# Optimization experiments

Hardware: AMD Instinct MI355X
Metric: run time of the kernel (lower is better)

The kernel has to match this reference:

```python
import jax, jax.numpy as jnp
import numpy as np

CUTOFF = 4          # lattice cutoff radius (module init arg)
NMAX = 64           # padded max neighbors per mobile site (~58 actual at cutoff=4)
BATCH = 131072      # number of independent configurations
B_SOFT = 0.01       # softening constant b in vint
FAR = 1e6           # padding position, masked out


def _rot(c):
    return np.array([[np.cos(c), -np.sin(c)], [np.sin(c), np.cos(c)]])


def _build_geometry():
    """Replicates PotEnergy1P.__init__ (with the intended, bug-fixed math)."""
    s3 = np.sqrt(3.0)
    base = [np.array([0.5, s3 / 6]), np.array([1.0, -s3 / 3]),
            np.array([1.5, s3 / 6]), np.array([1.0, 2 * s3 / 3])]
    mobile = base \
        + [_rot(2 * np.pi / 3) @ p for p in base] \
        + [_rot(4 * np.pi / 3) @ p for p in base]
    mobile = np.stack(mobile)                      # [12, 2]

    def ntopos(n1, n2):
        return np.array([0.5, s3 / 6]) + n1 * np.array([1.0, 0.0]) \
            + n2 * np.array([-0.5, s3 / 2])

    rng = range(-4 * CUTOFF, 4 * CUTOFF)
    grid = np.array([ntopos(n1, n2) for n1 in rng for n2 in rng])  # [G, 2]
    dist = np.linalg.norm(grid[:, None, :] - mobile[None, :, :], axis=-1)  # [G, 12]
    not_mobile = ~np.any(np.isclose(dist, 0.0, atol=1e-8), axis=1)        # [G]

    neighbors = np.full((12, NMAX, 2), FAR, dtype=np.float32)
    mask = np.zeros((12, NMAX), dtype=np.float32)
    for i in range(12):
        idx = np.where(not_mobile & (dist[:, i] < CUTOFF))[0]
        k = len(idx)
        assert k <= NMAX
        neighbors[i, :k] = grid[idx]
        mask[i, :k] = 1.0
    return neighbors, mask


def setup_inputs() -> dict:
    key = jax.random.key(0)
    x = jax.random.normal(key, (BATCH, 24), dtype=jnp.float32)
    neighbors, mask = _build_geometry()
    return {"x": x,
            "neighbors": jnp.asarray(neighbors),
            "mask": jnp.asarray(mask)}


def reference(x, neighbors, mask):
    # x: [B, 24] -> [B, 12, 2] mobile positions
    xr = x.reshape(x.shape[0], -1, 2)
    # pairwise displacement to all padded neighbors: [B, 12, NMAX, 2]
    d = xr[:, :, None, :] - neighbors[None, :, :, :]
    r = jnp.sqrt(jnp.sum(d * d, axis=-1))          # [B, 12, NMAX]
    v = jnp.exp(-r) / (r + B_SOFT)                 # vint with a=1.0, b=0.01
    return jnp.sum(v * mask[None], axis=(1, 2))    # [B] total potential energy
```

## Files before the change

### kernel.cpp

```cpp
#include <hip/hip_runtime.h>
#include <math.h>

#define NMAX   64
#define NSITES 12
#define SPLIT  4
#define BLOCK  256
#define RS     68

#define B_SOFT 0.01f
#define PAD_C  4.0e4f
#define R2_MAX 248.0f
#define TBL_LO 1392
#define TBL_N  768

#define NB_FLOATS  (NSITES * RS)
#define TBL_OFF    (TBL_LO * 8)
#define SMEM_BYTES (TBL_OFF + TBL_N * 8)

#define WS_TBL_F   1664
#define WS_FLOATS  3200
__device__ __align__(16) float g_ws[WS_FLOATS];
__device__ int g_m;

typedef float v2f __attribute__((ext_vector_type(2)));
typedef float v4f __attribute__((ext_vector_type(4)));

__device__ __forceinline__ float f_exact(float r2) {
    const float r = sqrtf(r2);
    return expf(-r) / (r + B_SOFT);
}

__global__ void init_kernel(const float* __restrict__ neighbors,
                            const float* __restrict__ mask) {
    __shared__ int cnt[NSITES];
    const int tid  = threadIdx.x;
    const int wv   = tid >> 6;
    const int lane = tid & 63;

    for (int i = tid; i < 2 * NB_FLOATS; i += BLOCK) g_ws[i] = PAD_C;
    __syncthreads();

    for (int s = wv; s < NSITES; s += 4) {
        const bool keep = mask[s * NMAX + lane] > 0.5f;
        const unsigned long long bal = __ballot(keep);
        if (keep) {
            const int pos = __popcll(bal & ((1ull << lane) - 1ull));
            const float2 p = ((const float2*)neighbors)[s * NMAX + lane];
            g_ws[s * RS + pos]             = p.x;
            g_ws[NB_FLOATS + s * RS + pos] = p.y;
        }
        if (lane == 0) cnt[s] = __popcll(bal);
    }
    __syncthreads();
    if (tid == 0) {
        int m = 0;
        #pragma unroll
        for (int s = 0; s < NSITES; ++s) m = max(m, cnt[s]);
        g_m = (m + 3) & ~3;
    }

    for (int i = tid; i < TBL_N; i += BLOCK) {
        const unsigned ii = (unsigned)(i + TBL_LO);
        const float b0 = __builtin_bit_cast(float, ii << 19);
        const float b1 = __builtin_bit_cast(float, (ii + 1u) << 19);
        const float f0 = f_exact(b0);
        const float f1 = f_exact(b1);
        const float fm = f_exact(0.5f * (b0 + b1));
        const float sl = (f1 - f0) / (b1 - b0);
        const float c  = f0 - sl * b0 - 0.5f * (0.5f * (f0 + f1) - fm);
        g_ws[WS_TBL_F + 2 * i]     = c;
        g_ws[WS_TBL_F + 2 * i + 1] = sl;
    }
}

__global__ __launch_bounds__(BLOCK, 8)
void pot_energy_kernel(const float* __restrict__ x,
                       float* __restrict__ out, int B) {
    __shared__ __align__(16) char smem[SMEM_BYTES];
    const int tid = threadIdx.x;

    {
        const float4* s0 = (const float4*)g_ws;
        float4* d0 = (float4*)smem;
        #pragma unroll
        for (int i = 0; i < 2; ++i) {
            const int idx = tid + i * BLOCK;
            if (idx < (2 * NB_FLOATS) / 4) d0[idx] = s0[idx];
        }
        const float4* s1 = (const float4*)(g_ws + WS_TBL_F);
        float4* d1 = (float4*)(smem + TBL_OFF);
        #pragma unroll
        for (int i = 0; i < 2; ++i) {
            const int idx = tid + i * BLOCK;
            if (idx < (TBL_N * 8) / 16) d1[idx] = s1[idx];
        }
    }
    const int m = g_m;
    __syncthreads();

    const int gtid = blockIdx.x * BLOCK + tid;
    const int e = gtid >> 2;
    const int q = gtid & 3;
    if (e >= B) return;

    const float2* xp = (const float2*)(x + (size_t)gtid * 6);
    const float2 p0 = xp[0], p1 = xp[1], p2 = xp[2];
    const float xs_[3] = { p0.x, p1.x, p2.x };
    const float ys_[3] = { p0.y, p1.y, p2.y };

    const float R2MINF = __builtin_bit_cast(float, 0x2B800000u);

    float accC = 0.f, accS = 0.f;
    #pragma unroll
    for (int s = 0; s < 3; ++s) {
        const int site = q * 3 + s;
        const float* __restrict__ rx = (const float*)smem + site * RS;
        const float* __restrict__ ry = rx + NB_FLOATS;
        const v2f xs2 = { xs_[s], xs_[s] };
        const v2f ys2 = { ys_[s], ys_[s] };
        #pragma unroll 2
        for (int j0 = 0; j0 < m; j0 += 4) {
            const v4f nx4 = *(const v4f*)(rx + j0);
            const v4f ny4 = *(const v4f*)(ry + j0);
            const v2f dxA = xs2 - nx4.xy;
            const v2f dxB = xs2 - nx4.zw;
            const v2f dyA = ys2 - ny4.xy;
            const v2f dyB = ys2 - ny4.zw;
            const v2f r2A = __builtin_elementwise_fma(dyA, dyA, dxA * dxA);
            const v2f r2B = __builtin_elementwise_fma(dyB, dyB, dxB * dxB);
            const float r2k[4] = { r2A.x, r2A.y, r2B.x, r2B.y };
            #pragma unroll
            for (int k = 0; k < 4; ++k) {
                const float r2c = __builtin_amdgcn_fmed3f(r2k[k], R2MINF, R2_MAX);
                const unsigned off =
                    (__builtin_bit_cast(unsigned, r2c) >> 16) & 0xFFF8u;
                const float2 cs = *(const float2*)(smem + off);
                accC += cs.x;
                accS = fmaf(cs.y, r2c, accS);
            }
        }
    }

    float acc = accC + accS;
    acc += __shfl_xor(acc, 1);
    acc += __shfl_xor(acc, 2);
    if (q == 0) out[e] = acc;
}

extern "C" void kernel_launch(void* const* d_in, const int* in_sizes, int n_in,
                              void* d_out, int out_size, void* d_ws, size_t ws_size,
                              hipStream_t stream) {
    const float* x   = (const float*)d_in[0];
    const float* nbr = (const float*)d_in[1];
    const float* msk = (const float*)d_in[2];
    float* out = (float*)d_out;

    const int B = in_sizes[0] / 24;

    init_kernel<<<1, BLOCK, 0, stream>>>(nbr, msk);

    const int total_threads = B * SPLIT;
    const int blocks = (total_threads + BLOCK - 1) / BLOCK;
    pot_energy_kernel<<<blocks, BLOCK, 0, stream>>>(x, out, B);
}
```

Baseline: 80.95 us.

## Replace piecewise-linear LDS lookup table with direct transcendental evaluation

Drops the precomputed interpolation table for exp(-r)/(r+b) indexed by r2 bits, and computes each pair term directly with hardware sqrt, exp2 and rcp intrinsics. This removes the per-pair LDS gather, with its possible bank conflicts, and the table build in the init kernel. In exchange each pair now issues three transcendental instructions, which run at reduced rate, and the packed v2f math is gone. Precision now relies on approximate rcp/exp instead of the table error.

After: 90.38 us. 1.12x slower.

```diff
diff --git a/kernel.cpp b/kernel.cpp
--- a/kernel.cpp
+++ b/kernel.cpp
@@ -9,26 +9,14 @@
 
 #define B_SOFT 0.01f
 #define PAD_C  4.0e4f
-#define R2_MAX 248.0f
-#define TBL_LO 1392
-#define TBL_N  768
 
-#define NB_FLOATS  (NSITES * RS)
-#define TBL_OFF    (TBL_LO * 8)
-#define SMEM_BYTES (TBL_OFF + TBL_N * 8)
+#define NB_FLOATS (NSITES * RS)
+#define WS_F      (2 * NB_FLOATS)
 
-#define WS_TBL_F   1664
-#define WS_FLOATS  3200
-__device__ __align__(16) float g_ws[WS_FLOATS];
+__device__ __align__(16) float g_ws[WS_F];
 __device__ int g_m;
 
-typedef float v2f __attribute__((ext_vector_type(2)));
 typedef float v4f __attribute__((ext_vector_type(4)));
-
-__device__ __forceinline__ float f_exact(float r2) {
-    const float r = sqrtf(r2);
-    return expf(-r) / (r + B_SOFT);
-}
 
 __global__ void init_kernel(const float* __restrict__ neighbors,
                             const float* __restrict__ mask) {
@@ -37,7 +25,7 @@
     const int wv   = tid >> 6;
     const int lane = tid & 63;
 
-    for (int i = tid; i < 2 * NB_FLOATS; i += BLOCK) g_ws[i] = PAD_C;
+    for (int i = tid; i < WS_F; i += BLOCK) g_ws[i] = PAD_C;
     __syncthreads();
 
     for (int s = wv; s < NSITES; s += 4) {
@@ -58,41 +46,21 @@
         for (int s = 0; s < NSITES; ++s) m = max(m, cnt[s]);
         g_m = (m + 3) & ~3;
     }
-
-    for (int i = tid; i < TBL_N; i += BLOCK) {
-        const unsigned ii = (unsigned)(i + TBL_LO);
-        const float b0 = __builtin_bit_cast(float, ii << 19);
-        const float b1 = __builtin_bit_cast(float, (ii + 1u) << 19);
-        const float f0 = f_exact(b0);
-        const float f1 = f_exact(b1);
-        const float fm = f_exact(0.5f * (b0 + b1));
-        const float sl = (f1 - f0) / (b1 - b0);
-        const float c  = f0 - sl * b0 - 0.5f * (0.5f * (f0 + f1) - fm);
-        g_ws[WS_TBL_F + 2 * i]     = c;
-        g_ws[WS_TBL_F + 2 * i + 1] = sl;
-    }
 }
 
 __global__ __launch_bounds__(BLOCK, 8)
 void pot_energy_kernel(const float* __restrict__ x,
                        float* __restrict__ out, int B) {
-    __shared__ __align__(16) char smem[SMEM_BYTES];
+    __shared__ __align__(16) float smem[WS_F];
     const int tid = threadIdx.x;
 
     {
-        const float4* s0 = (const float4*)g_ws;
-        float4* d0 = (float4*)smem;
+        const float4* s4 = (const float4*)g_ws;
+        float4* d4 = (float4*)smem;
         #pragma unroll
         for (int i = 0; i < 2; ++i) {
             const int idx = tid + i * BLOCK;
-            if (idx < (2 * NB_FLOATS) / 4) d0[idx] = s0[idx];
-        }
-        const float4* s1 = (const float4*)(g_ws + WS_TBL_F);
-        float4* d1 = (float4*)(smem + TBL_OFF);
-        #pragma unroll
-        for (int i = 0; i < 2; ++i) {
-            const int idx = tid + i * BLOCK;
-            if (idx < (TBL_N * 8) / 16) d1[idx] = s1[idx];
+            if (idx < WS_F / 4) d4[idx] = s4[idx];
         }
     }
     const int m = g_m;
@@ -108,40 +76,37 @@
     const float xs_[3] = { p0.x, p1.x, p2.x };
     const float ys_[3] = { p0.y, p1.y, p2.y };
 
-    const float R2MINF = __builtin_bit_cast(float, 0x2B800000u);
+    const float NLOG2E = -1.4426950408889634f;
 
-    float accC = 0.f, accS = 0.f;
+    float acc0 = 0.f, acc1 = 0.f;
     #pragma unroll
     for (int s = 0; s < 3; ++s) {
         const int site = q * 3 + s;
-        const float* __restrict__ rx = (const float*)smem + site * RS;
+        const float xs = xs_[s];
+        const float ys = ys_[s];
+        const float* __restrict__ rx = smem + site * RS;
         const float* __restrict__ ry = rx + NB_FLOATS;
-        const v2f xs2 = { xs_[s], xs_[s] };
-        const v2f ys2 = { ys_[s], ys_[s] };
         #pragma unroll 2
         for (int j0 = 0; j0 < m; j0 += 4) {
             const v4f nx4 = *(const v4f*)(rx + j0);
             const v4f ny4 = *(const v4f*)(ry + j0);
-            const v2f dxA = xs2 - nx4.xy;
-            const v2f dxB = xs2 - nx4.zw;
-            const v2f dyA = ys2 - ny4.xy;
-            const v2f dyB = ys2 - ny4.zw;
-            const v2f r2A = __builtin_elementwise_fma(dyA, dyA, dxA * dxA);
-            const v2f r2B = __builtin_elementwise_fma(dyB, dyB, dxB * dxB);
-            const float r2k[4] = { r2A.x, r2A.y, r2B.x, r2B.y };
+            const float nx[4] = { nx4.x, nx4.y, nx4.z, nx4.w };
+            const float ny[4] = { ny4.x, ny4.y, ny4.z, ny4.w };
             #pragma unroll
             for (int k = 0; k < 4; ++k) {
-                const float r2c = __builtin_amdgcn_fmed3f(r2k[k], R2MINF, R2_MAX);
-                const unsigned off =
-                    (__builtin_bit_cast(unsigned, r2c) >> 16) & 0xFFF8u;
-                const float2 cs = *(const float2*)(smem + off);
-                accC += cs.x;
-                accS = fmaf(cs.y, r2c, accS);
+                const float dx = xs - nx[k];
+                const float dy = ys - ny[k];
+                const float r2 = fmaf(dy, dy, dx * dx);
+                const float r  = __builtin_amdgcn_sqrtf(r2);
+                const float ex = __builtin_amdgcn_exp2f(r * NLOG2E);
+                const float rc = __builtin_amdgcn_rcpf(r + B_SOFT);
+                if (k & 1) acc1 = fmaf(ex, rc, acc1);
+                else       acc0 = fmaf(ex, rc, acc0);
             }
         }
     }
 
-    float acc = accC + accS;
+    float acc = acc0 + acc1;
     acc += __shfl_xor(acc, 1);
     acc += __shfl_xor(acc, 2);
     if (q == 0) out[e] = acc;
```

## Map site groups to wavefronts, drop clamp via padding/eps, reduce via LDS

Applied to the files above, without the earlier changes.

Each of the four wavefronts in a block now handles one group of three sites for the same 64 configurations, so the neighbor count is wave-uniform per group and the quarter split no longer needs lane shuffles. The final sum goes through LDS partials and a block barrier. The fmed3 clamp is removed by using a small padding coordinate and an epsilon term in r2, with the table extended so every index stays in range. The x loads become strided across lanes (24-float stride), which may reduce coalescing, and the extra barrier adds some sync cost.

Result: no change. 80.65 us (-0.4%).

```diff
diff --git a/kernel.cpp b/kernel.cpp
--- a/kernel.cpp
+++ b/kernel.cpp
@@ -3,24 +3,28 @@
 
 #define NMAX   64
 #define NSITES 12
-#define SPLIT  4
 #define BLOCK  256
+#define EPB    64
 #define RS     68
 
 #define B_SOFT 0.01f
-#define PAD_C  4.0e4f
-#define R2_MAX 248.0f
+#define PAD_C  14.0f
 #define TBL_LO 1392
-#define TBL_N  768
+#define TBL_N  800
+#define RAW_LO (TBL_LO * 8)
 
-#define NB_FLOATS  (NSITES * RS)
-#define TBL_OFF    (TBL_LO * 8)
-#define SMEM_BYTES (TBL_OFF + TBL_N * 8)
+#define NB_F   (NSITES * RS)
+#define GW_NBX (2 * TBL_N)
+#define GW_NBY (GW_NBX + NB_F)
+#define GW_F   (GW_NBY + NB_F)
 
-#define WS_TBL_F   1664
-#define WS_FLOATS  3200
-__device__ __align__(16) float g_ws[WS_FLOATS];
-__device__ int g_m;
+#define L_NBX  (2 * TBL_N)
+#define L_NBY  (L_NBX + NB_F)
+#define L_PART (L_NBY + NB_F)
+#define SMEM_F (L_PART + 3 * EPB)
+
+__device__ __align__(16) float g_ws[GW_F];
+__device__ int g_mq[4];
 
 typedef float v2f __attribute__((ext_vector_type(2)));
 typedef float v4f __attribute__((ext_vector_type(4)));
@@ -37,28 +41,6 @@
     const int wv   = tid >> 6;
     const int lane = tid & 63;
 
-    for (int i = tid; i < 2 * NB_FLOATS; i += BLOCK) g_ws[i] = PAD_C;
-    __syncthreads();
-
-    for (int s = wv; s < NSITES; s += 4) {
-        const bool keep = mask[s * NMAX + lane] > 0.5f;
-        const unsigned long long bal = __ballot(keep);
-        if (keep) {
-            const int pos = __popcll(bal & ((1ull << lane) - 1ull));
-            const float2 p = ((const float2*)neighbors)[s * NMAX + lane];
-            g_ws[s * RS + pos]             = p.x;
-            g_ws[NB_FLOATS + s * RS + pos] = p.y;
-        }
-        if (lane == 0) cnt[s] = __popcll(bal);
-    }
-    __syncthreads();
-    if (tid == 0) {
-        int m = 0;
-        #pragma unroll
-        for (int s = 0; s < NSITES; ++s) m = max(m, cnt[s]);
-        g_m = (m + 3) & ~3;
-    }
-
     for (int i = tid; i < TBL_N; i += BLOCK) {
         const unsigned ii = (unsigned)(i + TBL_LO);
         const float b0 = __builtin_bit_cast(float, ii << 19);
@@ -68,54 +50,72 @@
         const float fm = f_exact(0.5f * (b0 + b1));
         const float sl = (f1 - f0) / (b1 - b0);
         const float c  = f0 - sl * b0 - 0.5f * (0.5f * (f0 + f1) - fm);
-        g_ws[WS_TBL_F + 2 * i]     = c;
-        g_ws[WS_TBL_F + 2 * i + 1] = sl;
+        g_ws[2 * i]     = c;
+        g_ws[2 * i + 1] = sl;
+    }
+
+    for (int i = tid; i < 2 * NB_F; i += BLOCK) g_ws[GW_NBX + i] = PAD_C;
+    __syncthreads();
+
+    for (int s = wv; s < NSITES; s += 4) {
+        const bool keep = mask[s * NMAX + lane] > 0.5f;
+        const unsigned long long bal = __ballot(keep);
+        if (keep) {
+            const int pos = __popcll(bal & ((1ull << lane) - 1ull));
+            const float2 p = ((const float2*)neighbors)[s * NMAX + lane];
+            g_ws[GW_NBX + s * RS + pos] = p.x;
+            g_ws[GW_NBY + s * RS + pos] = p.y;
+        }
+        if (lane == 0) cnt[s] = __popcll(bal);
+    }
+    __syncthreads();
+    if (tid < 4) {
+        const int mm = max(cnt[3 * tid],
+                       max(cnt[3 * tid + 1], cnt[3 * tid + 2]));
+        g_mq[tid] = (mm + 3) & ~3;
     }
 }
 
 __global__ __launch_bounds__(BLOCK, 8)
 void pot_energy_kernel(const float* __restrict__ x,
                        float* __restrict__ out, int B) {
-    __shared__ __align__(16) char smem[SMEM_BYTES];
-    const int tid = threadIdx.x;
+    __shared__ __align__(16) float smem[SMEM_F];
+    const int tid  = threadIdx.x;
+    const int w    = tid >> 6;
+    const int lane = tid & 63;
 
     {
-        const float4* s0 = (const float4*)g_ws;
-        float4* d0 = (float4*)smem;
+        const float4* s4 = (const float4*)g_ws;
+        float4* d4 = (float4*)smem;
         #pragma unroll
-        for (int i = 0; i < 2; ++i) {
-            const int idx = tid + i * BLOCK;
-            if (idx < (2 * NB_FLOATS) / 4) d0[idx] = s0[idx];
-        }
-        const float4* s1 = (const float4*)(g_ws + WS_TBL_F);
-        float4* d1 = (float4*)(smem + TBL_OFF);
-        #pragma unroll
-        for (int i = 0; i < 2; ++i) {
-            const int idx = tid + i * BLOCK;
-            if (idx < (TBL_N * 8) / 16) d1[idx] = s1[idx];
+        for (int i0 = 0; i0 < 4; ++i0) {
+            const int i = tid + i0 * BLOCK;
+            if (i < GW_F / 4) d4[i] = s4[i];
         }
     }
-    const int m = g_m;
+    const int q = __builtin_amdgcn_readfirstlane(w);
+    const int m = g_mq[q];
     __syncthreads();
 
-    const int gtid = blockIdx.x * BLOCK + tid;
-    const int e = gtid >> 2;
-    const int q = gtid & 3;
-    if (e >= B) return;
+    const int e  = blockIdx.x * EPB + lane;
+    const int el = (e < B) ? e : 0;
 
-    const float2* xp = (const float2*)(x + (size_t)gtid * 6);
-    const float2 p0 = xp[0], p1 = xp[1], p2 = xp[2];
-    const float xs_[3] = { p0.x, p1.x, p2.x };
-    const float ys_[3] = { p0.y, p1.y, p2.y };
+    const float* xb = x + (size_t)el * 24 + q * 6;
+    const float2 pa = ((const float2*)xb)[0];
+    const float2 pb = ((const float2*)xb)[1];
+    const float2 pc = ((const float2*)xb)[2];
+    const float xs_[3] = { pa.x, pb.x, pc.x };
+    const float ys_[3] = { pa.y, pb.y, pc.y };
 
-    const float R2MINF = __builtin_bit_cast(float, 0x2B800000u);
+    const char* tb = (const char*)smem - RAW_LO;
+    const v2f eps2 = { 9.094947e-13f, 9.094947e-13f };
 
     float accC = 0.f, accS = 0.f;
     #pragma unroll
     for (int s = 0; s < 3; ++s) {
         const int site = q * 3 + s;
-        const float* __restrict__ rx = (const float*)smem + site * RS;
-        const float* __restrict__ ry = rx + NB_FLOATS;
+        const float* __restrict__ rx = smem + L_NBX + site * RS;
+        const float* __restrict__ ry = smem + L_NBY + site * RS;
         const v2f xs2 = { xs_[s], xs_[s] };
         const v2f ys2 = { ys_[s], ys_[s] };
         #pragma unroll 2
@@ -126,25 +126,30 @@
             const v2f dxB = xs2 - nx4.zw;
             const v2f dyA = ys2 - ny4.xy;
             const v2f dyB = ys2 - ny4.zw;
-            const v2f r2A = __builtin_elementwise_fma(dyA, dyA, dxA * dxA);
-            const v2f r2B = __builtin_elementwise_fma(dyB, dyB, dxB * dxB);
+            const v2f r2A = __builtin_elementwise_fma(
+                dyA, dyA, __builtin_elementwise_fma(dxA, dxA, eps2));
+            const v2f r2B = __builtin_elementwise_fma(
+                dyB, dyB, __builtin_elementwise_fma(dxB, dxB, eps2));
             const float r2k[4] = { r2A.x, r2A.y, r2B.x, r2B.y };
             #pragma unroll
             for (int k = 0; k < 4; ++k) {
-                const float r2c = __builtin_amdgcn_fmed3f(r2k[k], R2MINF, R2_MAX);
-                const unsigned off =
-                    (__builtin_bit_cast(unsigned, r2c) >> 16) & 0xFFF8u;
-                const float2 cs = *(const float2*)(smem + off);
+                const unsigned raw =
+                    (__builtin_bit_cast(unsigned, r2k[k]) >> 16) & 0xFFF8u;
+                const float2 cs = *(const float2*)(tb + raw);
                 accC += cs.x;
-                accS = fmaf(cs.y, r2c, accS);
+                accS = fmaf(cs.y, r2k[k], accS);
             }
         }
     }
 
-    float acc = accC + accS;
-    acc += __shfl_xor(acc, 1);
-    acc += __shfl_xor(acc, 2);
-    if (q == 0) out[e] = acc;
+    const float av = accC + accS;
+    if (w != 0) smem[L_PART + (w - 1) * EPB + lane] = av;
+    __syncthreads();
+    if (w == 0 && e < B) {
+        out[e] = av + smem[L_PART + lane]
+                    + smem[L_PART + EPB + lane]
+                    + smem[L_PART + 2 * EPB + lane];
+    }
 }
 
 extern "C" void kernel_launch(void* const* d_in, const int* in_sizes, int n_in,
@@ -159,7 +164,6 @@
 
     init_kernel<<<1, BLOCK, 0, stream>>>(nbr, msk);
 
-    const int total_threads = B * SPLIT;
-    const int blocks = (total_threads + BLOCK - 1) / BLOCK;
+    const int blocks = (B + EPB - 1) / EPB;
     pot_energy_kernel<<<blocks, BLOCK, 0, stream>>>(x, out, B);
 }
```
